# Kernel tuning notes

Hardware: AMD Instinct MI355X
Metric: run time of the kernel (lower is better)

The kernel has to match this reference:

```python
import jax, jax.numpy as jnp
import numpy as np

N_NODES = 20000
N_EDGES = 160000
CIN = 2000
N1 = 500
N2 = 250
DIM_Z = 16


def _xavier(key, shape):
    fan_out, fan_in = shape
    lim = jnp.sqrt(6.0 / (fan_in + fan_out))
    return jax.random.uniform(key, shape, jnp.float32, -lim, lim)


def setup_inputs() -> dict:
    key = jax.random.key(0)
    ks = jax.random.split(key, 10)
    data_in = jax.random.normal(ks[0], (N_NODES, CIN), jnp.float32)
    edge_index = jax.random.randint(ks[1], (2, N_EDGES), 0, N_NODES, jnp.int64)
    edge_weight = jax.random.uniform(ks[2], (N_EDGES,), jnp.float32)
    return {
        "data_in": data_in,
        "edge_index": edge_index,
        "edge_weight": edge_weight,
        "W1": _xavier(ks[3], (N1, CIN)),
        "b1": jnp.zeros((N1,), jnp.float32),
        "W2": _xavier(ks[4], (N2, N1)),
        "b2": jnp.zeros((N2,), jnp.float32),
        "W_mu_t": _xavier(ks[5], (1, N2)),
        "b_mu_t": jnp.zeros((1,), jnp.float32),
        "W_std_t": _xavier(ks[6], (1, N2)),
        "b_std_t": jnp.zeros((1,), jnp.float32),
        "W_mu_z": _xavier(ks[7], (DIM_Z, N2)),
        "b_mu_z": jnp.zeros((DIM_Z,), jnp.float32),
        "W_std_z": _xavier(ks[8], (DIM_Z, N2)),
        "b_std_z": jnp.zeros((DIM_Z,), jnp.float32),
    }


def gcn_conv(x, W, b, src, dst, ew, n_nodes):
    """PyG GCNConv: add self-loops (weight 1), symmetric deg^-1/2 normalization,
    linear transform, scatter-add aggregate to target nodes, add bias."""
    loop = jnp.arange(n_nodes, dtype=src.dtype)
    src_f = jnp.concatenate([src, loop])
    dst_f = jnp.concatenate([dst, loop])
    ew_f = jnp.concatenate([ew, jnp.ones((n_nodes,), ew.dtype)])
    deg = jax.ops.segment_sum(ew_f, dst_f, num_segments=n_nodes)
    dinv = jnp.where(deg > 0, jax.lax.rsqrt(deg), 0.0)
    norm = dinv[src_f] * ew_f * dinv[dst_f]  # [E+N]
    h = x @ W.T                               # [N, F_out]
    msgs = h[src_f] * norm[:, None]           # [E+N, F_out] gathered messages
    out = jax.ops.segment_sum(msgs, dst_f, num_segments=n_nodes)
    return out + b


def reference(data_in, edge_index, edge_weight, W1, b1, W2, b2,
              W_mu_t, b_mu_t, W_std_t, b_std_t, W_mu_z, b_mu_z, W_std_z, b_std_z):
    src, dst = edge_index[0], edge_index[1]
    n = data_in.shape[0]
    h = gcn_conv(data_in, W1, b1, src, dst, edge_weight, n)
    h = gcn_conv(h, W2, b2, src, dst, edge_weight, n)
    mu_tx = jax.nn.softplus(h @ W_mu_t.T + b_mu_t)
    std_tx = jax.nn.softplus(h @ W_std_t.T + b_std_t)
    mu_zx = h @ W_mu_z.T + b_mu_z
    std_zx = jax.nn.softplus(h @ W_std_z.T + b_std_z)
    return (mu_tx, std_tx, mu_zx, std_zx)
```

## Files before the change

kernel.cpp:

```cpp
#include <hip/hip_runtime.h>

#define N_NODES 20000
#define N_EDGES 160000
#define CIN     2000
#define N1      500
#define N2      250
#define NH      34
#define NHP     64

typedef __attribute__((ext_vector_type(4))) float f32x4;
typedef __attribute__((ext_vector_type(8))) __bf16 bf16x8;
typedef __attribute__((ext_vector_type(8))) unsigned short ushort8;

typedef const __attribute__((address_space(1))) void* as1cv;
typedef __attribute__((address_space(3))) void* as3v;

__device__ __forceinline__ unsigned short f2bf(float f) {
    unsigned int u = __builtin_bit_cast(unsigned int, f);
    u += 0x7FFFu + ((u >> 16) & 1u);
    return (unsigned short)(u >> 16);
}

__device__ __forceinline__ ushort8 pack8(float4 a, float4 b) {
    ushort8 r;
    r[0] = f2bf(a.x); r[1] = f2bf(a.y); r[2] = f2bf(a.z); r[3] = f2bf(a.w);
    r[4] = f2bf(b.x); r[5] = f2bf(b.y); r[6] = f2bf(b.z); r[7] = f2bf(b.w);
    return r;
}

__global__ __launch_bounds__(256) void k1(
    const int* __restrict__ ei, const float* __restrict__ ew,
    float* degsum, int* cnt,
    const float* __restrict__ W2,
    const float* __restrict__ Wmt, const float* __restrict__ Wst,
    const float* __restrict__ Wmz, const float* __restrict__ Wsz,
    float* __restrict__ V, unsigned short* __restrict__ Vb,
    const float* __restrict__ W1, unsigned short* __restrict__ W1T) {
    __shared__ float tile[32][33];
    const int B = blockIdx.x, t = threadIdx.x;
    if (B < 625) {
        int e = B * 256 + t;
        if (e < N_EDGES) {
            int d = ei[N_EDGES + e];
            atomicAdd(&degsum[d], ew[e]);
            atomicAdd(&cnt[d], 1);
        }
        return;
    }
    if (B < 753) {
        float* wh = &tile[0][0];
        int b = B - 625;
        int o = b >> 1, half = b & 1;
        int n = half * 256 + t;
        if (o >= NH) {
            V[(size_t)o * 512 + n] = 0.f;
            Vb[(size_t)o * 512 + n] = 0;
            return;
        }
        const float* src; int row;
        if (o == 0)      { src = Wmt; row = 0; }
        else if (o == 1) { src = Wst; row = 0; }
        else if (o < 18) { src = Wmz; row = o - 2; }
        else             { src = Wsz; row = o - 18; }
        if (t < N2) wh[t] = src[(size_t)row * N2 + t];
        __syncthreads();
        float acc = 0.f;
        if (n < N1) {
            for (int j = 0; j < N2; ++j) acc += wh[j] * W2[(size_t)j * N1 + n];
        }
        float v = (n < N1) ? acc : 0.f;
        V[(size_t)o * 512 + n] = v;
        Vb[(size_t)o * 512 + n] = f2bf(v);
        return;
    }
    int bb = B - 753;
    int jt = bb & 15, nt = bb >> 4;
    int c = t & 31, r = t >> 5;
#pragma unroll
    for (int i = 0; i < 4; ++i) {
        int j = jt * 32 + r + i * 8;
        int n = nt * 32 + c;
        tile[r + i * 8][c] = (j < N1 && n < CIN) ? W1[(size_t)j * CIN + n] : 0.f;
    }
    __syncthreads();
#pragma unroll
    for (int i = 0; i < 4; ++i) {
        int n = nt * 32 + r + i * 8;
        int j = jt * 32 + c;
        W1T[(size_t)n * 512 + j] = f2bf(tile[c][r + i * 8]);
    }
}

__global__ __launch_bounds__(256) void k2(
    const int* __restrict__ cnt, const float* __restrict__ degsum,
    float* __restrict__ dinv, int* __restrict__ rowPtr, int* __restrict__ cursor,
    const unsigned short* __restrict__ Vb, const unsigned short* __restrict__ W1T,
    unsigned short* __restrict__ Wtb,
    const float* __restrict__ V,
    const float* __restrict__ b1, const float* __restrict__ b2,
    const float* __restrict__ bmt, const float* __restrict__ bst,
    const float* __restrict__ bmz, const float* __restrict__ bsz,
    const float* __restrict__ Wmt, const float* __restrict__ Wst,
    const float* __restrict__ Wmz, const float* __restrict__ Wsz,
    float* __restrict__ ccdd) {
    __shared__ alignas(16) unsigned short lA[128 * 32];
    __shared__ alignas(16) unsigned short lB[128 * 32];
    __shared__ int sdata[256];
    const int B = blockIdx.x, t = threadIdx.x;
    if (B < 79) {
        const int nbase = B * 256;
        int idx = nbase + t;
        if (idx < N_NODES) cursor[idx] = 0;
        int s = 0;
        for (int i = t; i < nbase; i += 256) s += cnt[i];
        sdata[t] = s;
        __syncthreads();
        for (int off = 128; off; off >>= 1) {
            if (t < off) sdata[t] += sdata[t + off];
            __syncthreads();
        }
        const int base = sdata[0];
        __syncthreads();
        int v = 0;
        if (idx < N_NODES) {
            v = cnt[idx];
            dinv[idx] = rsqrtf(1.0f + degsum[idx]);
        }
        sdata[t] = v;
        __syncthreads();
        for (int off = 1; off < 256; off <<= 1) {
            int x = (t >= off) ? sdata[t - off] : 0;
            __syncthreads();
            sdata[t] += x;
            __syncthreads();
        }
        if (idx < N_NODES) rowPtr[idx] = base + sdata[t] - v;
        if (B == 78 && t == 255) rowPtr[N_NODES] = base + sdata[255];
        return;
    }
    if (B == 79) {
        int w = t >> 6, lane = t & 63;
        for (int o = w; o < NH; o += 4) {
            float cc = 0.f;
            for (int n = lane; n < N1; n += 64) cc += V[(size_t)o * 512 + n] * b1[n];
            const float* src; int row; float bias;
            if (o == 0)      { src = Wmt; row = 0;      bias = bmt[0]; }
            else if (o == 1) { src = Wst; row = 0;      bias = bst[0]; }
            else if (o < 18) { src = Wmz; row = o - 2;  bias = bmz[o - 2]; }
            else             { src = Wsz; row = o - 18; bias = bsz[o - 18]; }
            float dd = 0.f;
            for (int j = lane; j < N2; j += 64) dd += src[(size_t)row * N2 + j] * b2[j];
#pragma unroll
            for (int off = 32; off; off >>= 1) {
                cc += __shfl_down(cc, off);
                dd += __shfl_down(dd, off);
            }
            if (lane == 0) { ccdd[o] = cc; ccdd[NHP + o] = dd + bias; }
        }
        if (t >= NH && t < NHP) { ccdd[t] = 0.f; ccdd[NHP + t] = 0.f; }
        return;
    }
    {
        const int w = t >> 6, lane = t & 63;
        const int bn0 = (B - 80) * 128;
        const int M = 64;
        const int wr = w >> 1, wc = w & 1;
        const int lr = lane & 15, lk = (lane >> 4) * 8;
        f32x4 acc[4][4];
#pragma unroll
        for (int i = 0; i < 4; i++)
#pragma unroll
            for (int j = 0; j < 4; j++) acc[i][j] = (f32x4){0.f, 0.f, 0.f, 0.f};
        for (int kt = 0; kt < 16; ++kt) {
            const int kb = kt * 32;
#pragma unroll
            for (int i = 0; i < 2; i++) {
                int c0 = i * 256 + w * 64;
                int c  = c0 + lane;
                int rr = c >> 2, kg = c & 3;
                int grow = rr < M ? rr : M - 1;
                const unsigned short* gp = Vb + (size_t)grow * 512 + kb + kg * 8;
                __builtin_amdgcn_global_load_lds((as1cv)gp, (as3v)(lA + (size_t)c0 * 8), 16, 0, 0);
            }
#pragma unroll
            for (int i = 0; i < 2; i++) {
                int c0 = i * 256 + w * 64;
                int c  = c0 + lane;
                int rr = c >> 2, kg = c & 3;
                const unsigned short* gp = W1T + (size_t)(bn0 + rr) * 512 + kb + kg * 8;
                __builtin_amdgcn_global_load_lds((as1cv)gp, (as3v)(lB + (size_t)c0 * 8), 16, 0, 0);
            }
            __syncthreads();
            ushort8 af[4], bfr[4];
#pragma unroll
            for (int m = 0; m < 4; m++)
                af[m] = *reinterpret_cast<const ushort8*>(&lA[(wr * 64 + m * 16 + lr) * 32 + lk]);
#pragma unroll
            for (int n = 0; n < 4; n++)
                bfr[n] = *reinterpret_cast<const ushort8*>(&lB[(wc * 64 + n * 16 + lr) * 32 + lk]);
#pragma unroll
            for (int m = 0; m < 4; m++)
#pragma unroll
                for (int n = 0; n < 4; n++)
                    acc[m][n] = __builtin_amdgcn_mfma_f32_16x16x32_bf16(
                        __builtin_bit_cast(bf16x8, af[m]), __builtin_bit_cast(bf16x8, bfr[n]),
                        acc[m][n], 0, 0, 0);
            __syncthreads();
        }
        const int crow0 = wr * 64 + (lane >> 4) * 4;
        const int ccol0 = bn0 + wc * 64 + lr;
#pragma unroll
        for (int m = 0; m < 4; m++)
#pragma unroll
            for (int n = 0; n < 4; n++)
#pragma unroll
                for (int rg = 0; rg < 4; rg++) {
                    int row = crow0 + m * 16 + rg;
                    if (row < M)
                        Wtb[(size_t)row * 2048 + ccol0 + n * 16] = f2bf(acc[m][n][rg]);
                }
    }
}

__global__ __launch_bounds__(256) void k3(
    const float* __restrict__ X, const unsigned short* __restrict__ Wtb,
    float* __restrict__ Tpart,
    const int* __restrict__ ei, const float* __restrict__ ew,
    const float* __restrict__ dinv, const int* __restrict__ rowPtr,
    int* cursor, int* __restrict__ colA, float* __restrict__ valA) {
    __shared__ alignas(16) unsigned short lA[64 * 64];
    __shared__ alignas(16) unsigned short lB[64 * 64];
    const int B = blockIdx.x, t = threadIdx.x;
    if (B >= 626) {
        int e = (B - 626) * 256 + t;
        if (e < N_EDGES) {
            int s = ei[e], d = ei[N_EDGES + e];
            int p = atomicAdd(&cursor[d], 1);
            int j = rowPtr[d] + p;
            colA[j] = s;
            valA[j] = dinv[s] * ew[e] * dinv[d];
        }
        return;
    }
    const int w = t >> 6, lane = t & 63;
    const int kp = B & 1;
    const int bm0 = (B >> 1) * 64;
    const int kbase = kp * 1024;
    const int lr = lane & 15, lkb = (lane >> 4) * 16;

    const int c0 = t, c1 = t + 256;
    const int ar0 = c0 >> 3, ac0 = (c0 & 7) * 8;
    const int ar1 = c1 >> 3, ac1 = (c1 & 7) * 8;
    int gr0 = bm0 + ar0; if (gr0 >= N_NODES) gr0 = N_NODES - 1;
    int gr1 = bm0 + ar1; if (gr1 >= N_NODES) gr1 = N_NODES - 1;
    const float* pA0 = X + (size_t)gr0 * CIN + kbase + ac0;
    const float* pA1 = X + (size_t)gr1 * CIN + kbase + ac1;
    const unsigned short* pB0 = Wtb + ar0 * 2048 + kbase + ac0;
    const unsigned short* pB1 = Wtb + ar1 * 2048 + kbase + ac1;
    char* const LA = (char*)lA;
    char* const LB = (char*)lB;
    char* const wA0 = LA + ((ar0 * 128 + ac0 * 2) ^ ((ar0 & 7) << 4));
    char* const wA1 = LA + ((ar1 * 128 + ac1 * 2) ^ ((ar1 & 7) << 4));
    char* const wB0 = LB + ((ar0 * 128 + ac0 * 2) ^ ((ar0 & 7) << 4));
    char* const wB1 = LB + ((ar1 * 128 + ac1 * 2) ^ ((ar1 & 7) << 4));

    int aoff[4][2], boff[2];
#pragma unroll
    for (int m = 0; m < 4; ++m)
#pragma unroll
        for (int k = 0; k < 2; ++k)
            aoff[m][k] = (((m * 16 + lr) * 128 + k * 64 + lkb) ^ ((lr & 7) << 4));
#pragma unroll
    for (int k = 0; k < 2; ++k)
        boff[k] = (((w * 16 + lr) * 128 + k * 64 + lkb) ^ ((lr & 7) << 4));

    f32x4 acc[4];
#pragma unroll
    for (int m = 0; m < 4; ++m) acc[m] = (f32x4){0.f, 0.f, 0.f, 0.f};

    float4 a00A, a01A, a10A, a11A; ushort8 bv0A, bv1A;
    float4 a00B, a01B, a10B, a11B; ushort8 bv0B, bv1B;
    const float4 z4 = make_float4(0.f, 0.f, 0.f, 0.f);

#define STAGE_LOAD(S, a00_, a01_, a10_, a11_, bv0_, bv1_)                          \
    {                                                                              \
        bool v0 = (kbase + ac0 + (S) * 64) < CIN;                                  \
        bool v1 = (kbase + ac1 + (S) * 64) < CIN;                                  \
        const float4* q0 = (const float4*)(v0 ? pA0 + (S) * 64 : (const float*)X); \
        const float4* q1 = (const float4*)(v1 ? pA1 + (S) * 64 : (const float*)X); \
        a00_ = q0[0]; a01_ = q0[1];                                                \
        a10_ = q1[0]; a11_ = q1[1];                                                \
        if (!v0) { a00_ = z4; a01_ = z4; }                                         \
        if (!v1) { a10_ = z4; a11_ = z4; }                                         \
        bv0_ = *(const ushort8*)(pB0 + (S) * 64);                                  \
        bv1_ = *(const ushort8*)(pB1 + (S) * 64);                                  \
    }

    auto compute = [&]() {
#pragma unroll
        for (int k = 0; k < 2; ++k) {
            ushort8 bf = *(const ushort8*)(LB + boff[k]);
#pragma unroll
            for (int m = 0; m < 4; ++m) {
                ushort8 af = *(const ushort8*)(LA + aoff[m][k]);
                acc[m] = __builtin_amdgcn_mfma_f32_16x16x32_bf16(
                    __builtin_bit_cast(bf16x8, af), __builtin_bit_cast(bf16x8, bf),
                    acc[m], 0, 0, 0);
            }
        }
    };

    STAGE_LOAD(0, a00A, a01A, a10A, a11A, bv0A, bv1A)
    STAGE_LOAD(1, a00B, a01B, a10B, a11B, bv0B, bv1B)
    for (int s2 = 0; s2 < 8; ++s2) {
        const int s = 2 * s2;
        __syncthreads();
        *(ushort8*)wA0 = pack8(a00A, a01A);
        *(ushort8*)wA1 = pack8(a10A, a11A);
        *(ushort8*)wB0 = bv0A;
        *(ushort8*)wB1 = bv1A;
        __syncthreads();
        if (s + 2 < 16) STAGE_LOAD(s + 2, a00A, a01A, a10A, a11A, bv0A, bv1A)
        compute();
        __syncthreads();
        *(ushort8*)wA0 = pack8(a00B, a01B);
        *(ushort8*)wA1 = pack8(a10B, a11B);
        *(ushort8*)wB0 = bv0B;
        *(ushort8*)wB1 = bv1B;
        __syncthreads();
        if (s + 3 < 16) STAGE_LOAD(s + 3, a00B, a01B, a10B, a11B, bv0B, bv1B)
        compute();
    }
#undef STAGE_LOAD
    float* Tp = Tpart + (size_t)kp * N_NODES * NHP;
    const int col = w * 16 + lr;
    const int rb = bm0 + (lane >> 4) * 4;
#pragma unroll
    for (int m = 0; m < 4; ++m)
#pragma unroll
        for (int rg = 0; rg < 4; ++rg) {
            int row = rb + m * 16 + rg;
            if (row < N_NODES) Tp[(size_t)row * NHP + col] = acc[m][rg];
        }
}

__global__ __launch_bounds__(256) void agg_a(
    const float* __restrict__ Tp, const int* __restrict__ rowPtr,
    const int* __restrict__ colA, const float* __restrict__ valA,
    const float* __restrict__ dinv, float* __restrict__ U) {
    const float* __restrict__ T1 = Tp + (size_t)N_NODES * NHP;
    int wid = blockIdx.x * 4 + (threadIdx.x >> 6);
    int lane = threadIdx.x & 63;
    if (wid >= N_NODES) return;
    int d = wid;
    float dv = dinv[d];
    float acc = dv * dv * (Tp[(size_t)d * NHP + lane] + T1[(size_t)d * NHP + lane]);
    int e0 = rowPtr[d], e1 = rowPtr[d + 1];
    int e = e0;
    for (; e + 8 <= e1; e += 8) {
        int   s0 = colA[e],     s1 = colA[e + 1], s2 = colA[e + 2], s3 = colA[e + 3];
        int   s4 = colA[e + 4], s5 = colA[e + 5], s6 = colA[e + 6], s7 = colA[e + 7];
        float w0 = valA[e],     w1 = valA[e + 1], w2 = valA[e + 2], w3 = valA[e + 3];
        float w4 = valA[e + 4], w5 = valA[e + 5], w6 = valA[e + 6], w7 = valA[e + 7];
        float t0 = Tp[(size_t)s0 * NHP + lane] + T1[(size_t)s0 * NHP + lane];
        float t1 = Tp[(size_t)s1 * NHP + lane] + T1[(size_t)s1 * NHP + lane];
        float t2 = Tp[(size_t)s2 * NHP + lane] + T1[(size_t)s2 * NHP + lane];
        float t3 = Tp[(size_t)s3 * NHP + lane] + T1[(size_t)s3 * NHP + lane];
        float t4 = Tp[(size_t)s4 * NHP + lane] + T1[(size_t)s4 * NHP + lane];
        float t5 = Tp[(size_t)s5 * NHP + lane] + T1[(size_t)s5 * NHP + lane];
        float t6 = Tp[(size_t)s6 * NHP + lane] + T1[(size_t)s6 * NHP + lane];
        float t7 = Tp[(size_t)s7 * NHP + lane] + T1[(size_t)s7 * NHP + lane];
        acc += w0 * t0 + w1 * t1 + w2 * t2 + w3 * t3
             + w4 * t4 + w5 * t5 + w6 * t6 + w7 * t7;
    }
    for (; e + 4 <= e1; e += 4) {
        int s0 = colA[e], s1 = colA[e + 1], s2 = colA[e + 2], s3 = colA[e + 3];
        float w0 = valA[e], w1 = valA[e + 1], w2 = valA[e + 2], w3 = valA[e + 3];
        float t0 = Tp[(size_t)s0 * NHP + lane] + T1[(size_t)s0 * NHP + lane];
        float t1 = Tp[(size_t)s1 * NHP + lane] + T1[(size_t)s1 * NHP + lane];
        float t2 = Tp[(size_t)s2 * NHP + lane] + T1[(size_t)s2 * NHP + lane];
        float t3 = Tp[(size_t)s3 * NHP + lane] + T1[(size_t)s3 * NHP + lane];
        acc += w0 * t0 + w1 * t1 + w2 * t2 + w3 * t3;
    }
    for (; e < e1; ++e) {
        int s = colA[e];
        acc += valA[e] * (Tp[(size_t)s * NHP + lane] + T1[(size_t)s * NHP + lane]);
    }
    U[(size_t)d * NHP + lane] = acc;
}

__global__ __launch_bounds__(256) void agg_b(
    const float* __restrict__ U, const int* __restrict__ rowPtr,
    const int* __restrict__ colA, const float* __restrict__ valA,
    const float* __restrict__ dinv, const float* __restrict__ ccdd,
    float* __restrict__ out) {
    int wid = blockIdx.x * 4 + (threadIdx.x >> 6);
    int lane = threadIdx.x & 63;
    if (wid >= N_NODES) return;
    int d = wid;
    float dv = dinv[d], self = dv * dv;
    float acc = self * U[(size_t)d * NHP + lane];
    float r = self;
    int e0 = rowPtr[d], e1 = rowPtr[d + 1];
    int e = e0;
    for (; e + 8 <= e1; e += 8) {
        int   s0 = colA[e],     s1 = colA[e + 1], s2 = colA[e + 2], s3 = colA[e + 3];
        int   s4 = colA[e + 4], s5 = colA[e + 5], s6 = colA[e + 6], s7 = colA[e + 7];
        float w0 = valA[e],     w1 = valA[e + 1], w2 = valA[e + 2], w3 = valA[e + 3];
        float w4 = valA[e + 4], w5 = valA[e + 5], w6 = valA[e + 6], w7 = valA[e + 7];
        float t0 = U[(size_t)s0 * NHP + lane], t1 = U[(size_t)s1 * NHP + lane];
        float t2 = U[(size_t)s2 * NHP + lane], t3 = U[(size_t)s3 * NHP + lane];
        float t4 = U[(size_t)s4 * NHP + lane], t5 = U[(size_t)s5 * NHP + lane];
        float t6 = U[(size_t)s6 * NHP + lane], t7 = U[(size_t)s7 * NHP + lane];
        acc += w0 * t0 + w1 * t1 + w2 * t2 + w3 * t3
             + w4 * t4 + w5 * t5 + w6 * t6 + w7 * t7;
        r += w0 + w1 + w2 + w3 + w4 + w5 + w6 + w7;
    }
    for (; e + 4 <= e1; e += 4) {
        int s0 = colA[e], s1 = colA[e + 1], s2 = colA[e + 2], s3 = colA[e + 3];
        float w0 = valA[e], w1 = valA[e + 1], w2 = valA[e + 2], w3 = valA[e + 3];
        float t0 = U[(size_t)s0 * NHP + lane], t1 = U[(size_t)s1 * NHP + lane];
        float t2 = U[(size_t)s2 * NHP + lane], t3 = U[(size_t)s3 * NHP + lane];
        acc += w0 * t0 + w1 * t1 + w2 * t2 + w3 * t3;
        r += w0 + w1 + w2 + w3;
    }
    for (; e < e1; ++e) {
        int s = colA[e];
        float wv = valA[e];
        acc += wv * U[(size_t)s * NHP + lane];
        r += wv;
    }
    if (lane < NH) {
        float v = acc + r * ccdd[lane] + ccdd[NHP + lane];
        if (lane < 2 || lane >= 18)
            v = fmaxf(v, 0.f) + log1pf(expf(-fabsf(v)));
        size_t oidx;
        if (lane == 0)      oidx = (size_t)d;
        else if (lane == 1) oidx = (size_t)N_NODES + d;
        else if (lane < 18) oidx = (size_t)2 * N_NODES + (size_t)d * 16 + (lane - 2);
        else                oidx = (size_t)18 * N_NODES + (size_t)d * 16 + (lane - 18);
        out[oidx] = v;
    }
}

extern "C" void kernel_launch(void* const* d_in, const int* in_sizes, int n_in,
                              void* d_out, int out_size, void* d_ws, size_t ws_size,
                              hipStream_t stream) {
    const float* X   = (const float*)d_in[0];
    const int*   EI  = (const int*)d_in[1];
    const float* EW  = (const float*)d_in[2];
    const float* W1  = (const float*)d_in[3];
    const float* b1  = (const float*)d_in[4];
    const float* W2  = (const float*)d_in[5];
    const float* b2  = (const float*)d_in[6];
    const float* Wmt = (const float*)d_in[7];
    const float* bmt = (const float*)d_in[8];
    const float* Wst = (const float*)d_in[9];
    const float* bst = (const float*)d_in[10];
    const float* Wmz = (const float*)d_in[11];
    const float* bmz = (const float*)d_in[12];
    const float* Wsz = (const float*)d_in[13];
    const float* bsz = (const float*)d_in[14];
    float* out = (float*)d_out;

    char* ws = (char*)d_ws;
    size_t off = 0;
    auto alloc = [&](size_t bytes) -> char* {
        char* p = ws + off;
        off += (bytes + 255) & ~(size_t)255;
        return p;
    };
    float*          V    = (float*)alloc((size_t)NHP * 512 * 4);
    unsigned short* Vb   = (unsigned short*)alloc((size_t)NHP * 512 * 2);
    unsigned short* W1T  = (unsigned short*)alloc((size_t)2048 * 512 * 2);
    unsigned short* Wtb  = (unsigned short*)alloc((size_t)NHP * 2048 * 2);
    float*          ccdd = (float*)alloc(2 * NHP * 4);
    float*          Tp   = (float*)alloc((size_t)2 * N_NODES * NHP * 4);
    float*          U    = (float*)alloc((size_t)N_NODES * NHP * 4);
    float* degsum = (float*)alloc(N_NODES * 4);
    int*   cnt    = (int*)alloc(N_NODES * 4);
    int*   cursor = (int*)alloc(N_NODES * 4);
    float* dinv   = (float*)alloc(N_NODES * 4);
    int*   rowPtr = (int*)alloc((N_NODES + 1) * 4);
    int*   colA   = (int*)alloc(N_EDGES * 4);
    float* valA   = (float*)alloc(N_EDGES * 4);
    if (off > ws_size) return;

    size_t zspan = (size_t)((char*)(cnt + N_NODES) - (char*)degsum);
    hipMemsetAsync(degsum, 0, zspan, stream);

    k1<<<625 + 128 + 1024, 256, 0, stream>>>(EI, EW, degsum, cnt,
                                             W2, Wmt, Wst, Wmz, Wsz, V, Vb, W1, W1T);
    k2<<<79 + 1 + 16, 256, 0, stream>>>(cnt, degsum, dinv, rowPtr, cursor,
                                        Vb, W1T, Wtb, V,
                                        b1, b2, bmt, bst, bmz, bsz, Wmt, Wst, Wmz, Wsz, ccdd);
    k3<<<626 + 625, 256, 0, stream>>>(X, Wtb, Tp, EI, EW, dinv, rowPtr, cursor, colA, valA);
    agg_a<<<(N_NODES + 3) / 4, 256, 0, stream>>>(Tp, rowPtr, colA, valA, dinv, U);
    agg_b<<<(N_NODES + 3) / 4, 256, 0, stream>>>(U, rowPtr, colA, valA, dinv, ccdd, out);
}
```

Baseline: 123.5 us.

## Replace split-K GEMM tiling with 32-row full-K tiles and single output buffer

```diff
diff --git a/kernel.cpp b/kernel.cpp
--- a/kernel.cpp
+++ b/kernel.cpp
@@ -66,7 +66,17 @@
         __syncthreads();
         float acc = 0.f;
         if (n < N1) {
-            for (int j = 0; j < N2; ++j) acc += wh[j] * W2[(size_t)j * N1 + n];
+            const float* p = W2 + n;
+            int j = 0;
+            for (; j + 8 <= N2; j += 8) {
+                float x0 = p[(size_t)(j + 0) * N1], x1 = p[(size_t)(j + 1) * N1];
+                float x2 = p[(size_t)(j + 2) * N1], x3 = p[(size_t)(j + 3) * N1];
+                float x4 = p[(size_t)(j + 4) * N1], x5 = p[(size_t)(j + 5) * N1];
+                float x6 = p[(size_t)(j + 6) * N1], x7 = p[(size_t)(j + 7) * N1];
+                acc += wh[j] * x0 + wh[j + 1] * x1 + wh[j + 2] * x2 + wh[j + 3] * x3
+                     + wh[j + 4] * x4 + wh[j + 5] * x5 + wh[j + 6] * x6 + wh[j + 7] * x7;
+            }
+            for (; j < N2; ++j) acc += wh[j] * p[(size_t)j * N1];
         }
         float v = (n < N1) ? acc : 0.f;
         V[(size_t)o * 512 + n] = v;
@@ -224,15 +234,15 @@
 
 __global__ __launch_bounds__(256) void k3(
     const float* __restrict__ X, const unsigned short* __restrict__ Wtb,
-    float* __restrict__ Tpart,
+    float* __restrict__ T,
     const int* __restrict__ ei, const float* __restrict__ ew,
     const float* __restrict__ dinv, const int* __restrict__ rowPtr,
     int* cursor, int* __restrict__ colA, float* __restrict__ valA) {
-    __shared__ alignas(16) unsigned short lA[64 * 64];
+    __shared__ alignas(16) unsigned short lA[32 * 64];
     __shared__ alignas(16) unsigned short lB[64 * 64];
     const int B = blockIdx.x, t = threadIdx.x;
-    if (B >= 626) {
-        int e = (B - 626) * 256 + t;
+    if (B >= 625) {
+        int e = (B - 625) * 256 + t;
         if (e < N_EDGES) {
             int s = ei[e], d = ei[N_EDGES + e];
             int p = atomicAdd(&cursor[d], 1);
@@ -243,30 +253,24 @@
         return;
     }
     const int w = t >> 6, lane = t & 63;
-    const int kp = B & 1;
-    const int bm0 = (B >> 1) * 64;
-    const int kbase = kp * 1024;
+    const int bm0 = B * 32;
     const int lr = lane & 15, lkb = (lane >> 4) * 16;
 
-    const int c0 = t, c1 = t + 256;
-    const int ar0 = c0 >> 3, ac0 = (c0 & 7) * 8;
-    const int ar1 = c1 >> 3, ac1 = (c1 & 7) * 8;
-    int gr0 = bm0 + ar0; if (gr0 >= N_NODES) gr0 = N_NODES - 1;
-    int gr1 = bm0 + ar1; if (gr1 >= N_NODES) gr1 = N_NODES - 1;
-    const float* pA0 = X + (size_t)gr0 * CIN + kbase + ac0;
-    const float* pA1 = X + (size_t)gr1 * CIN + kbase + ac1;
-    const unsigned short* pB0 = Wtb + ar0 * 2048 + kbase + ac0;
-    const unsigned short* pB1 = Wtb + ar1 * 2048 + kbase + ac1;
+    const int arow = t >> 3, acol = (t & 7) * 8;
+    const int b0r = t >> 3, b0c = (t & 7) * 8;
+    const int b1r = (t >> 3) + 32, b1c = (t & 7) * 8;
+    const float* pA = X + (size_t)(bm0 + arow) * CIN + acol;
+    const unsigned short* pB0 = Wtb + (size_t)b0r * 2048 + b0c;
+    const unsigned short* pB1 = Wtb + (size_t)b1r * 2048 + b1c;
     char* const LA = (char*)lA;
     char* const LB = (char*)lB;
-    char* const wA0 = LA + ((ar0 * 128 + ac0 * 2) ^ ((ar0 & 7) << 4));
-    char* const wA1 = LA + ((ar1 * 128 + ac1 * 2) ^ ((ar1 & 7) << 4));
-    char* const wB0 = LB + ((ar0 * 128 + ac0 * 2) ^ ((ar0 & 7) << 4));
-    char* const wB1 = LB + ((ar1 * 128 + ac1 * 2) ^ ((ar1 & 7) << 4));
-
-    int aoff[4][2], boff[2];
-#pragma unroll
-    for (int m = 0; m < 4; ++m)
+    char* const wA  = LA + ((arow * 128 + acol * 2) ^ ((arow & 7) << 4));
+    char* const wB0 = LB + ((b0r * 128 + b0c * 2) ^ ((b0r & 7) << 4));
+    char* const wB1 = LB + ((b1r * 128 + b1c * 2) ^ ((b1r & 7) << 4));
+
+    int aoff[2][2], boff[2];
+#pragma unroll
+    for (int m = 0; m < 2; ++m)
 #pragma unroll
         for (int k = 0; k < 2; ++k)
             aoff[m][k] = (((m * 16 + lr) * 128 + k * 64 + lkb) ^ ((lr & 7) << 4));
@@ -274,26 +278,22 @@
     for (int k = 0; k < 2; ++k)
         boff[k] = (((w * 16 + lr) * 128 + k * 64 + lkb) ^ ((lr & 7) << 4));
 
-    f32x4 acc[4];
-#pragma unroll
-    for (int m = 0; m < 4; ++m) acc[m] = (f32x4){0.f, 0.f, 0.f, 0.f};
-
-    float4 a00A, a01A, a10A, a11A; ushort8 bv0A, bv1A;
-    float4 a00B, a01B, a10B, a11B; ushort8 bv0B, bv1B;
+    f32x4 acc[2];
+    acc[0] = (f32x4){0.f, 0.f, 0.f, 0.f};
+    acc[1] = (f32x4){0.f, 0.f, 0.f, 0.f};
+
+    float4 aAx, aAy; ushort8 bA0, bA1;
+    float4 aBx, aBy; ushort8 bB0, bB1;
     const float4 z4 = make_float4(0.f, 0.f, 0.f, 0.f);
 
-#define STAGE_LOAD(S, a00_, a01_, a10_, a11_, bv0_, bv1_)                          \
+#define STAGE_LOAD(S, ax_, ay_, b0_, b1_)                                          \
     {                                                                              \
-        bool v0 = (kbase + ac0 + (S) * 64) < CIN;                                  \
-        bool v1 = (kbase + ac1 + (S) * 64) < CIN;                                  \
-        const float4* q0 = (const float4*)(v0 ? pA0 + (S) * 64 : (const float*)X); \
-        const float4* q1 = (const float4*)(v1 ? pA1 + (S) * 64 : (const float*)X); \
-        a00_ = q0[0]; a01_ = q0[1];                                                \
-        a10_ = q1[0]; a11_ = q1[1];                                                \
-        if (!v0) { a00_ = z4; a01_ = z4; }                                         \
-        if (!v1) { a10_ = z4; a11_ = z4; }                                         \
-        bv0_ = *(const ushort8*)(pB0 + (S) * 64);                                  \
-        bv1_ = *(const ushort8*)(pB1 + (S) * 64);                                  \
+        bool va = ((S) * 64 + acol) < CIN;                                         \
+        const float4* q = (const float4*)(va ? pA + (S) * 64 : (const float*)X);   \
+        ax_ = q[0]; ay_ = q[1];                                                    \
+        if (!va) { ax_ = z4; ay_ = z4; }                                           \
+        b0_ = *(const ushort8*)(pB0 + (S) * 64);                                   \
+        b1_ = *(const ushort8*)(pB1 + (S) * 64);                                   \
     }
 
     auto compute = [&]() {
@@ -301,7 +301,7 @@
         for (int k = 0; k < 2; ++k) {
             ushort8 bf = *(const ushort8*)(LB + boff[k]);
 #pragma unroll
-            for (int m = 0; m < 4; ++m) {
+            for (int m = 0; m < 2; ++m) {
                 ushort8 af = *(const ushort8*)(LA + aoff[m][k]);
                 acc[m] = __builtin_amdgcn_mfma_f32_16x16x32_bf16(
                     __builtin_bit_cast(bf16x8, af), __builtin_bit_cast(bf16x8, bf),
@@ -310,51 +310,45 @@
         }
     };
 
-    STAGE_LOAD(0, a00A, a01A, a10A, a11A, bv0A, bv1A)
-    STAGE_LOAD(1, a00B, a01B, a10B, a11B, bv0B, bv1B)
-    for (int s2 = 0; s2 < 8; ++s2) {
+    STAGE_LOAD(0, aAx, aAy, bA0, bA1)
+    STAGE_LOAD(1, aBx, aBy, bB0, bB1)
+    for (int s2 = 0; s2 < 16; ++s2) {
         const int s = 2 * s2;
         __syncthreads();
-        *(ushort8*)wA0 = pack8(a00A, a01A);
-        *(ushort8*)wA1 = pack8(a10A, a11A);
-        *(ushort8*)wB0 = bv0A;
-        *(ushort8*)wB1 = bv1A;
-        __syncthreads();
-        if (s + 2 < 16) STAGE_LOAD(s + 2, a00A, a01A, a10A, a11A, bv0A, bv1A)
+        *(ushort8*)wA  = pack8(aAx, aAy);
+        *(ushort8*)wB0 = bA0;
+        *(ushort8*)wB1 = bA1;
+        __syncthreads();
+        if (s + 2 < 32) STAGE_LOAD(s + 2, aAx, aAy, bA0, bA1)
         compute();
         __syncthreads();
-        *(ushort8*)wA0 = pack8(a00B, a01B);
-        *(ushort8*)wA1 = pack8(a10B, a11B);
-        *(ushort8*)wB0 = bv0B;
-        *(ushort8*)wB1 = bv1B;
-        __syncthreads();
-        if (s + 3 < 16) STAGE_LOAD(s + 3, a00B, a01B, a10B, a11B, bv0B, bv1B)
+        *(ushort8*)wA  = pack8(aBx, aBy);
+        *(ushort8*)wB0 = bB0;
+        *(ushort8*)wB1 = bB1;
+        __syncthreads();
+        if (s + 3 < 32) STAGE_LOAD(s + 3, aBx, aBy, bB0, bB1)
         compute();
     }
 #undef STAGE_LOAD
-    float* Tp = Tpart + (size_t)kp * N_NODES * NHP;
     const int col = w * 16 + lr;
     const int rb = bm0 + (lane >> 4) * 4;
 #pragma unroll
-    for (int m = 0; m < 4; ++m)
-#pragma unroll
-        for (int rg = 0; rg < 4; ++rg) {
-            int row = rb + m * 16 + rg;
-            if (row < N_NODES) Tp[(size_t)row * NHP + col] = acc[m][rg];
-        }
+    for (int m = 0; m < 2; ++m)
+#pragma unroll
+        for (int rg = 0; rg < 4; ++rg)
+            T[(size_t)(rb + m * 16 + rg) * NHP + col] = acc[m][rg];
 }
 
 __global__ __launch_bounds__(256) void agg_a(
-    const float* __restrict__ Tp, const int* __restrict__ rowPtr,
+    const float* __restrict__ T, const int* __restrict__ rowPtr,
     const int* __restrict__ colA, const float* __restrict__ valA,
     const float* __restrict__ dinv, float* __restrict__ U) {
-    const float* __restrict__ T1 = Tp + (size_t)N_NODES * NHP;
     int wid = blockIdx.x * 4 + (threadIdx.x >> 6);
     int lane = threadIdx.x & 63;
     if (wid >= N_NODES) return;
     int d = wid;
     float dv = dinv[d];
-    float acc = dv * dv * (Tp[(size_t)d * NHP + lane] + T1[(size_t)d * NHP + lane]);
+    float acc = dv * dv * T[(size_t)d * NHP + lane];
     int e0 = rowPtr[d], e1 = rowPtr[d + 1];
     int e = e0;
     for (; e + 8 <= e1; e += 8) {
@@ -362,29 +356,16 @@
         int   s4 = colA[e + 4], s5 = colA[e + 5], s6 = colA[e + 6], s7 = colA[e + 7];
         float w0 = valA[e],     w1 = valA[e + 1], w2 = valA[e + 2], w3 = valA[e + 3];
         float w4 = valA[e + 4], w5 = valA[e + 5], w6 = valA[e + 6], w7 = valA[e + 7];
-        float t0 = Tp[(size_t)s0 * NHP + lane] + T1[(size_t)s0 * NHP + lane];
-        float t1 = Tp[(size_t)s1 * NHP + lane] + T1[(size_t)s1 * NHP + lane];
-        float t2 = Tp[(size_t)s2 * NHP + lane] + T1[(size_t)s2 * NHP + lane];
-        float t3 = Tp[(size_t)s3 * NHP + lane] + T1[(size_t)s3 * NHP + lane];
-        float t4 = Tp[(size_t)s4 * NHP + lane] + T1[(size_t)s4 * NHP + lane];
-        float t5 = Tp[(size_t)s5 * NHP + lane] + T1[(size_t)s5 * NHP + lane];
-        float t6 = Tp[(size_t)s6 * NHP + lane] + T1[(size_t)s6 * NHP + lane];
-        float t7 = Tp[(size_t)s7 * NHP + lane] + T1[(size_t)s7 * NHP + lane];
+        float t0 = T[(size_t)s0 * NHP + lane], t1 = T[(size_t)s1 * NHP + lane];
+        float t2 = T[(size_t)s2 * NHP + lane], t3 = T[(size_t)s3 * NHP + lane];
+        float t4 = T[(size_t)s4 * NHP + lane], t5 = T[(size_t)s5 * NHP + lane];
+        float t6 = T[(size_t)s6 * NHP + lane], t7 = T[(size_t)s7 * NHP + lane];
         acc += w0 * t0 + w1 * t1 + w2 * t2 + w3 * t3
              + w4 * t4 + w5 * t5 + w6 * t6 + w7 * t7;
     }
-    for (; e + 4 <= e1; e += 4) {
-        int s0 = colA[e], s1 = colA[e + 1], s2 = colA[e + 2], s3 = colA[e + 3];
-        float w0 = valA[e], w1 = valA[e + 1], w2 = valA[e + 2], w3 = valA[e + 3];
-        float t0 = Tp[(size_t)s0 * NHP + lane] + T1[(size_t)s0 * NHP + lane];
-        float t1 = Tp[(size_t)s1 * NHP + lane] + T1[(size_t)s1 * NHP + lane];
-        float t2 = Tp[(size_t)s2 * NHP + lane] + T1[(size_t)s2 * NHP + lane];
-        float t3 = Tp[(size_t)s3 * NHP + lane] + T1[(size_t)s3 * NHP + lane];
-        acc += w0 * t0 + w1 * t1 + w2 * t2 + w3 * t3;
-    }
     for (; e < e1; ++e) {
         int s = colA[e];
-        acc += valA[e] * (Tp[(size_t)s * NHP + lane] + T1[(size_t)s * NHP + lane]);
+        acc += valA[e] * T[(size_t)s * NHP + lane];
     }
     U[(size_t)d * NHP + lane] = acc;
 }
@@ -416,14 +397,6 @@
              + w4 * t4 + w5 * t5 + w6 * t6 + w7 * t7;
         r += w0 + w1 + w2 + w3 + w4 + w5 + w6 + w7;
     }
-    for (; e + 4 <= e1; e += 4) {
-        int s0 = colA[e], s1 = colA[e + 1], s2 = colA[e + 2], s3 = colA[e + 3];
-        float w0 = valA[e], w1 = valA[e + 1], w2 = valA[e + 2], w3 = valA[e + 3];
-        float t0 = U[(size_t)s0 * NHP + lane], t1 = U[(size_t)s1 * NHP + lane];
-        float t2 = U[(size_t)s2 * NHP + lane], t3 = U[(size_t)s3 * NHP + lane];
-        acc += w0 * t0 + w1 * t1 + w2 * t2 + w3 * t3;
-        r += w0 + w1 + w2 + w3;
-    }
     for (; e < e1; ++e) {
         int s = colA[e];
         float wv = valA[e];
@@ -475,7 +448,7 @@
     unsigned short* W1T  = (unsigned short*)alloc((size_t)2048 * 512 * 2);
     unsigned short* Wtb  = (unsigned short*)alloc((size_t)NHP * 2048 * 2);
     float*          ccdd = (float*)alloc(2 * NHP * 4);
-    float*          Tp   = (float*)alloc((size_t)2 * N_NODES * NHP * 4);
+    float*          T    = (float*)alloc((size_t)N_NODES * NHP * 4);
     float*          U    = (float*)alloc((size_t)N_NODES * NHP * 4);
     float* degsum = (float*)alloc(N_NODES * 4);
     int*   cnt    = (int*)alloc(N_NODES * 4);
@@ -494,7 +467,7 @@
     k2<<<79 + 1 + 16, 256, 0, stream>>>(cnt, degsum, dinv, rowPtr, cursor,
                                         Vb, W1T, Wtb, V,
                                         b1, b2, bmt, bst, bmz, bsz, Wmt, Wst, Wmz, Wsz, ccdd);
-    k3<<<626 + 625, 256, 0, stream>>>(X, Wtb, Tp, EI, EW, dinv, rowPtr, cursor, colA, valA);
-    agg_a<<<(N_NODES + 3) / 4, 256, 0, stream>>>(Tp, rowPtr, colA, valA, dinv, U);
+    k3<<<625 + 625, 256, 0, stream>>>(X, Wtb, T, EI, EW, dinv, rowPtr, cursor, colA, valA);
+    agg_a<<<(N_NODES + 3) / 4, 256, 0, stream>>>(T, rowPtr, colA, valA, dinv, U);
     agg_b<<<(N_NODES + 3) / 4, 256, 0, stream>>>(U, rowPtr, colA, valA, dinv, ccdd, out);
 }
```

After: 129.0 us. 1.04x slower.
